# Kernel tuning notes

Hardware: AMD Instinct MI355X
Metric: run time of the kernel (lower is better)

The kernel has to match this reference:

```python
import jax, jax.numpy as jnp
import numpy as np

B, C, H, W = 64, 3, 512, 512
P = 16
D = P * P          # 256 = patch_size**2 (token dim)
GH, GW = H // P, W // P
NP = GH * GW       # 1024 patches
HID = 1024         # FFN hidden
L = 6              # num_layers
NC = 1000          # num_classes
EPS = 1e-5


def setup_inputs() -> dict:
    key = jax.random.key(0)
    ks = jax.random.split(key, 8)
    n = lambda i, shape, scale=0.02: jax.random.normal(ks[i], shape, jnp.float32) * scale
    return dict(
        x=jax.random.normal(ks[0], (B, C, H, W), jnp.float32),
        conv_w=n(1, (D, C, P, P)),
        conv_b=jnp.zeros((D,), jnp.float32),
        pos_emb=n(2, (1, NP + 1, D), 1.0),
        cls_tok=n(3, (1, 1, D), 1.0),
        ln1_s=jnp.ones((L, D), jnp.float32), ln1_b=jnp.zeros((L, D), jnp.float32),
        ln2_s=jnp.ones((L, D), jnp.float32), ln2_b=jnp.zeros((L, D), jnp.float32),
        w1=n(4, (L, D, HID)), b1=jnp.zeros((L, HID), jnp.float32),
        w2=n(5, (L, HID, D)), b2=jnp.zeros((L, D), jnp.float32),
        head_ln_s=jnp.ones((D,), jnp.float32), head_ln_b=jnp.zeros((D,), jnp.float32),
        head_w=n(6, (D, NC)), head_b=jnp.zeros((NC,), jnp.float32),
    )


def _ln(x, s, b):
    m = x.mean(-1, keepdims=True)
    v = ((x - m) ** 2).mean(-1, keepdims=True)
    return (x - m) * jax.lax.rsqrt(v + EPS) * s + b


def reference(x, conv_w, conv_b, pos_emb, cls_tok,
              ln1_s, ln1_b, ln2_s, ln2_b, w1, b1, w2, b2,
              head_ln_s, head_ln_b, head_w, head_b):
    b = x.shape[0]
    # patch-embed conv (kernel==stride) as reshape + einsum
    xr = x.reshape(b, C, GH, P, GW, P)
    tok = jnp.einsum('bchpwq,dcpq->bhwd', xr, conv_w).reshape(b, NP, D) + conv_b
    t = jnp.concatenate([jnp.broadcast_to(cls_tok, (b, 1, D)), tok], axis=1) + pos_emb
    for i in range(L):
        # FNet token mixing: real part of 2D FFT over (tokens, dim)
        h = _ln(t, ln1_s[i], ln1_b[i])
        t = t + jnp.fft.fft2(h, axes=(-2, -1)).real
        # FFN
        h = _ln(t, ln2_s[i], ln2_b[i])
        h = jax.nn.leaky_relu(h @ w1[i] + b1[i], negative_slope=0.01) @ w2[i] + b2[i]
        t = t + h
    pooled = t.mean(axis=1)
    logits = _ln(pooled, head_ln_s, head_ln_b) @ head_w + head_b
    return jax.nn.softmax(logits, axis=-1)
```

## Files before the change

kernel.cpp:

```cpp
#include <hip/hip_runtime.h>
#include <math.h>

#define BATCH 64
#define CIN 3
#define IMH 512
#define IMW 512
#define PSZ 16
#define DIM 256
#define GHN 32
#define GWN 32
#define NTOK 1025
#define HID 1024
#define NLAYER 6
#define NCLS 1000
#define LN_EPS 1e-5f

#define KF 576
#define KR 640
#define MF 144
#define MROWS 65600

typedef __attribute__((ext_vector_type(8))) short short8;
typedef __attribute__((ext_vector_type(4))) float f32x4;

#define MFMA16(acc, a, b) acc = __builtin_amdgcn_mfma_f32_16x16x32_bf16(a, b, acc, 0, 0, 0)

__device__ inline unsigned short rne_bf16(float x) {
    unsigned u = __float_as_uint(x);
    return (unsigned short)((u + 0x7FFF + ((u >> 16) & 1)) >> 16);
}
__device__ inline void split_bf16(float x, unsigned short& hi, unsigned short& lo) {
    unsigned short h = rne_bf16(x);
    hi = h;
    float hf = __uint_as_float((unsigned)h << 16);
    lo = rne_bf16(x - hf);
}
__device__ inline float wave_sum(float v) {
#pragma unroll
    for (int off = 32; off; off >>= 1) v += __shfl_xor(v, off);
    return v;
}
__device__ inline short8 ld8x64(const unsigned short* lds, int row, int q) {
    return *(const short8*)(lds + (row * 8 + (q ^ (row & 7))) * 8);
}
__device__ inline short8 ld8x32(const unsigned short* lds, int row, int q) {
    return *(const short8*)(lds + (row * 4 + (q ^ ((row >> 1) & 3))) * 8);
}
__device__ inline void gl2lds16(const unsigned short* g, unsigned short* l) {
    __builtin_amdgcn_global_load_lds((const __attribute__((address_space(1))) unsigned int*)g,
                                     (__attribute__((address_space(3))) unsigned int*)l, 16, 0, 0);
}
__device__ inline void a_stage128(unsigned short* lds, const unsigned short* g, int lda, int tid, int maxrow) {
    int lane = tid & 63, w = tid >> 6;
#pragma unroll
    for (int s = 0; s < 4; s++) {
        int slot = w * 256 + s * 64;
        int sl = slot + lane;
        int row = sl >> 3, gc = (sl & 7) ^ (row & 7);
        if (row > maxrow) row = maxrow;
        gl2lds16(g + (size_t)row * lda + gc * 8, lds + slot * 8);
    }
}
__device__ inline void a_stage144x32(unsigned short* lds, const unsigned short* g, int lda, int tid) {
    int lane = tid & 63, w = tid >> 6;
#pragma unroll
    for (int s = 0; s < 2; s++) {
        int slot = s * 256 + w * 64;
        int sl = slot + lane;
        int row = sl >> 2, gc = (sl & 3) ^ ((row >> 1) & 3);
        gl2lds16(g + (size_t)row * lda + gc * 8, lds + slot * 8);
    }
    if (w == 0) {
        int slot = 512;
        int sl = slot + lane;
        int row = sl >> 2, gc = (sl & 3) ^ ((row >> 1) & 3);
        gl2lds16(g + (size_t)row * lda + gc * 8, lds + slot * 8);
    }
}

__global__ __launch_bounds__(256) void gen_dft2(unsigned short* C1h, unsigned short* C1l,
                                                unsigned short* S1h, unsigned short* S1l,
                                                unsigned short* C2h, unsigned short* C2l,
                                                unsigned short* S2h, unsigned short* S2l) {
    int idx = blockIdx.x * 256 + threadIdx.x;
    if (idx < KR * KF) {
        int k = idx / KF, n = idx - k * KF;
        float c = 0.f, s = 0.f;
        if (k <= 512 && n <= 512) {
            int r = (k * n) % 1025;
            double ang = 6.283185307179586476925287 * (double)r / 1025.0;
            c = (float)cos(ang); s = (float)sin(ang);
        }
        unsigned short h, l;
        split_bf16(c, h, l); C1h[idx] = h; C1l[idx] = l;
        split_bf16(s, h, l); S1h[idx] = h; S1l[idx] = l;
    }
    if (idx < 256 * 256) {
        int k = idx >> 8, n = idx & 255;
        int r = (k * n) & 255;
        double ang = 6.283185307179586476925287 * (double)r / 256.0;
        float c = (float)cos(ang), s = (float)sin(ang);
        unsigned short h, l;
        split_bf16(c, h, l); C2h[idx] = h; C2l[idx] = l;
        split_bf16(s, h, l); S2h[idx] = h; S2l[idx] = l;
    }
}

__global__ __launch_bounds__(256) void conv_wp(const float* __restrict__ w,
                                               unsigned short* __restrict__ wph, unsigned short* __restrict__ wpl) {
    int idx = blockIdx.x * 256 + threadIdx.x;
    unsigned short h, l;
    split_bf16(w[idx], h, l);
    wph[idx] = h; wpl[idx] = l;
}
__global__ __launch_bounds__(256) void conv_w1t(const float* __restrict__ w1, unsigned short* __restrict__ w1t) {
    int idx = blockIdx.x * 256 + threadIdx.x;
    int l = idx / 262144, rem = idx - l * 262144;
    int n = rem >> 8, k = rem & 255;
    w1t[idx] = rne_bf16(w1[(size_t)l * 262144 + (size_t)k * 1024 + n]);
}
__global__ __launch_bounds__(256) void conv_w2t(const float* __restrict__ w2, unsigned short* __restrict__ w2t) {
    int idx = blockIdx.x * 256 + threadIdx.x;
    int l = idx / 262144, rem = idx - l * 262144;
    int n = rem >> 10, k = rem & 1023;
    w2t[idx] = rne_bf16(w2[(size_t)l * 262144 + (size_t)k * 256 + n]);
}

__global__ __launch_bounds__(256) void cls_init(const float* __restrict__ cls, const float* __restrict__ pos,
                                                float* __restrict__ t) {
    int b = blockIdx.x, tid = threadIdx.x;
    t[(size_t)b * NTOK * DIM + tid] = cls[tid] + pos[tid];
}

__global__ __launch_bounds__(256) void patch_fused(const float* __restrict__ x,
                                                   const unsigned short* __restrict__ wph,
                                                   const unsigned short* __restrict__ wpl,
                                                   const float* __restrict__ cb, const float* __restrict__ pos,
                                                   float* __restrict__ t) {
    __shared__ __align__(16) unsigned short sAh[8192], sAl[8192], sBh[8192], sBl[8192];
    int m0 = blockIdx.x * 128, n0 = blockIdx.y * 128;
    int tid = threadIdx.x, lane = tid & 63, w = tid >> 6;
    int wr = (w >> 1) * 64, wc = (w & 1) * 64;
    f32x4 z = {0.f, 0.f, 0.f, 0.f};
    f32x4 acc[4][4] = {{z, z, z, z}, {z, z, z, z}, {z, z, z, z}, {z, z, z, z}};
    for (int k0 = 0; k0 < 768; k0 += 64) {
#pragma unroll
        for (int s = 0; s < 8; s++) {
            int lin = s * 1024 + tid * 4;
            int row = lin >> 6, kc = lin & 63;
            int m = m0 + row;
            int bb = m >> 10, gh = (m >> 5) & 31, gw = m & 31;
            int k = k0 + kc;
            int c = k >> 8, pp = (k >> 4) & 15, q = k & 15;
            const float* gp = x + (size_t)bb * 786432 + c * 262144 + gh * 8192 + pp * 512 + gw * 16 + q;
            float4 v = *(const float4*)gp;
            ushort4 oh, ol;
            split_bf16(v.x, oh.x, ol.x); split_bf16(v.y, oh.y, ol.y);
            split_bf16(v.z, oh.z, ol.z); split_bf16(v.w, oh.w, ol.w);
            int g = kc >> 3, half = (kc >> 2) & 1;
            int addr = (row * 8 + (g ^ (row & 7))) * 8 + half * 4;
            *(ushort4*)(sAh + addr) = oh;
            *(ushort4*)(sAl + addr) = ol;
        }
        a_stage128(sBh, wph + (size_t)n0 * 768 + k0, 768, tid, 127);
        a_stage128(sBl, wpl + (size_t)n0 * 768 + k0, 768, tid, 127);
        __syncthreads();
#pragma unroll
        for (int kc2 = 0; kc2 < 2; kc2++) {
            int q = (lane >> 4) + kc2 * 4;
            short8 ah[4], al[4], bh8[4], bl8[4];
#pragma unroll
            for (int i = 0; i < 4; i++) {
                ah[i] = ld8x64(sAh, wr + i * 16 + (lane & 15), q);
                al[i] = ld8x64(sAl, wr + i * 16 + (lane & 15), q);
                bh8[i] = ld8x64(sBh, wc + i * 16 + (lane & 15), q);
                bl8[i] = ld8x64(sBl, wc + i * 16 + (lane & 15), q);
            }
#pragma unroll
            for (int i = 0; i < 4; i++)
#pragma unroll
                for (int j = 0; j < 4; j++) {
                    MFMA16(acc[i][j], ah[i], bh8[j]);
                    MFMA16(acc[i][j], ah[i], bl8[j]);
                    MFMA16(acc[i][j], al[i], bh8[j]);
                }
        }
        __syncthreads();
    }
    int q4 = (lane >> 4) * 4;
#pragma unroll
    for (int i = 0; i < 4; i++) {
        int r = m0 + wr + i * 16 + q4;
#pragma unroll
        for (int j = 0; j < 4; j++) {
            int c = n0 + wc + j * 16 + (lane & 15);
#pragma unroll
            for (int g = 0; g < 4; g++) {
                int rr = r + g;
                int bb = rr >> 10, tok = 1 + (rr & 1023);
                t[((size_t)bb * NTOK + tok) * 256 + c] =
                    acc[i][j][g] + cb[c] + pos[(size_t)tok * 256 + c];
            }
        }
    }
}

__global__ __launch_bounds__(256) void ln_stats(const float* __restrict__ t, float2* __restrict__ stats) {
    int wave = threadIdx.x >> 6, lane = threadIdx.x & 63;
    int m = blockIdx.x * 4 + wave;
    const float* row = t + (size_t)m * DIM;
    float4 v = *(const float4*)(row + lane * 4);
    float mean = wave_sum(v.x + v.y + v.z + v.w) * (1.f / 256.f);
    float dx = v.x - mean, dy = v.y - mean, dz = v.z - mean, dw = v.w - mean;
    float sq = wave_sum(dx * dx + dy * dy + dz * dz + dw * dw);
    float rstd = rsqrtf(sq * (1.f / 256.f) + LN_EPS);
    if (lane == 0) stats[m] = make_float2(mean, rstd);
}

__global__ __launch_bounds__(256) void ln2_bf16(const float* __restrict__ t, unsigned short* __restrict__ hh,
                                                const float* __restrict__ s, const float* __restrict__ bb) {
    int wave = threadIdx.x >> 6, lane = threadIdx.x & 63;
    int m = blockIdx.x * 4 + wave;
    const float* row = t + (size_t)m * DIM;
    float4 v = *(const float4*)(row + lane * 4);
    float mean = wave_sum(v.x + v.y + v.z + v.w) * (1.f / 256.f);
    float dx = v.x - mean, dy = v.y - mean, dz = v.z - mean, dw = v.w - mean;
    float sq = wave_sum(dx * dx + dy * dy + dz * dz + dw * dw);
    float rstd = rsqrtf(sq * (1.f / 256.f) + LN_EPS);
    float4 s4 = *(const float4*)(s + lane * 4);
    float4 b4 = *(const float4*)(bb + lane * 4);
    ushort4 o;
    o.x = rne_bf16(dx * rstd * s4.x + b4.x);
    o.y = rne_bf16(dy * rstd * s4.y + b4.y);
    o.z = rne_bf16(dz * rstd * s4.z + b4.z);
    o.w = rne_bf16(dw * rstd * s4.w + b4.w);
    *(ushort4*)(hh + (size_t)m * DIM + lane * 4) = o;
}

__global__ __launch_bounds__(256) void fold_gemm(
    const float* __restrict__ tt, const float2* __restrict__ stats,
    const float* __restrict__ ls, const float* __restrict__ lb,
    const unsigned short* __restrict__ C2h, const unsigned short* __restrict__ C2l,
    const unsigned short* __restrict__ S2h, const unsigned short* __restrict__ S2l,
    unsigned short* __restrict__ Ycth, unsigned short* __restrict__ Yctl,
    unsigned short* __restrict__ Ysth, unsigned short* __restrict__ Ystl) {
    __shared__ __align__(16) unsigned short sAh[4096], sAl[4096], sBh[4608], sBl[4608];
    int m0 = blockIdx.x * 128;
    int zz = blockIdx.y;
    const unsigned short* Bh = zz ? S2h : C2h;
    const unsigned short* Bl = zz ? S2l : C2l;
    unsigned short* Oh = zz ? Ysth : Ycth;
    unsigned short* Ol = zz ? Ystl : Yctl;
    int tid = threadIdx.x, lane = tid & 63, w = tid >> 6;
    int wr = w * 32;
    f32x4 zf = {0.f, 0.f, 0.f, 0.f};
    f32x4 acc[2][9];
#pragma unroll
    for (int i = 0; i < 2; i++)
#pragma unroll
        for (int j = 0; j < 9; j++) acc[i][j] = zf;
    for (int k0 = 0; k0 < 256; k0 += 32) {
#pragma unroll
        for (int s = 0; s < 4; s++) {
            int sl = tid + s * 256;
            int row = sl >> 3, g = sl & 7;
            int r = m0 + row;
            int b = r / KF, np = r - b * KF;
            float4 hv = {0.f, 0.f, 0.f, 0.f};
            if (np <= 512) {
                int d0 = k0 + g * 4;
                float4 s4 = *(const float4*)(ls + d0);
                float4 b4 = *(const float4*)(lb + d0);
                int i1 = b * NTOK + np;
                float2 st1 = stats[i1];
                float4 va = *(const float4*)(tt + (size_t)i1 * 256 + d0);
                float hax = (va.x - st1.x) * st1.y * s4.x + b4.x;
                float hay = (va.y - st1.x) * st1.y * s4.y + b4.y;
                float haz = (va.z - st1.x) * st1.y * s4.z + b4.z;
                float haw = (va.w - st1.x) * st1.y * s4.w + b4.w;
                float hbx = 0.f, hby = 0.f, hbz = 0.f, hbw = 0.f;
                if (np >= 1) {
                    int i2 = b * NTOK + (NTOK - np);
                    float2 st2 = stats[i2];
                    float4 vb = *(const float4*)(tt + (size_t)i2 * 256 + d0);
                    hbx = (vb.x - st2.x) * st2.y * s4.x + b4.x;
                    hby = (vb.y - st2.x) * st2.y * s4.y + b4.y;
                    hbz = (vb.z - st2.x) * st2.y * s4.z + b4.z;
                    hbw = (vb.w - st2.x) * st2.y * s4.w + b4.w;
                }
                if (zz) { hv.x = hax - hbx; hv.y = hay - hby; hv.z = haz - hbz; hv.w = haw - hbw; }
                else    { hv.x = hax + hbx; hv.y = hay + hby; hv.z = haz + hbz; hv.w = haw + hbw; }
            }
            ushort4 oh, ol;
            split_bf16(hv.x, oh.x, ol.x); split_bf16(hv.y, oh.y, ol.y);
            split_bf16(hv.z, oh.z, ol.z); split_bf16(hv.w, oh.w, ol.w);
            int addr = (row * 4 + ((g >> 1) ^ ((row >> 1) & 3))) * 8 + (g & 1) * 4;
            *(ushort4*)(sAh + addr) = oh;
            *(ushort4*)(sAl + addr) = ol;
        }
        a_stage144x32(sBh, Bh + k0, 256, tid);
        a_stage144x32(sBl, Bl + k0, 256, tid);
        __syncthreads();
        int q = lane >> 4;
        short8 ah[2], al[2];
#pragma unroll
        for (int i = 0; i < 2; i++) {
            int r = wr + i * 16 + (lane & 15);
            ah[i] = ld8x32(sAh, r, q); al[i] = ld8x32(sAl, r, q);
        }
#pragma unroll
        for (int j = 0; j < 9; j++) {
            int rb = j * 16 + (lane & 15);
            short8 bh = ld8x32(sBh, rb, q), bl = ld8x32(sBl, rb, q);
#pragma unroll
            for (int i = 0; i < 2; i++) {
                MFMA16(acc[i][j], ah[i], bh);
                MFMA16(acc[i][j], ah[i], bl);
                MFMA16(acc[i][j], al[i], bh);
            }
        }
        __syncthreads();
    }
    int q4 = (lane >> 4) * 4;
#pragma unroll
    for (int i = 0; i < 2; i++) {
        int r = m0 + wr + i * 16 + q4;
        int bidx = r / KF, kp = r - bidx * KF;
#pragma unroll
        for (int j = 0; j < 9; j++) {
            int c = j * 16 + (lane & 15);
            ushort4 oh, ol;
            split_bf16(acc[i][j][0], oh.x, ol.x);
            split_bf16(acc[i][j][1], oh.y, ol.y);
            split_bf16(acc[i][j][2], oh.z, ol.z);
            split_bf16(acc[i][j][3], oh.w, ol.w);
            size_t off = ((size_t)bidx * MF + c) * KF + kp;
            *(ushort4*)(Oh + off) = oh;
            *(ushort4*)(Ol + off) = ol;
        }
    }
}

__global__ __launch_bounds__(512, 6) void fft_big_dual(
    const unsigned short* __restrict__ C1h, const unsigned short* __restrict__ C1l,
    const unsigned short* __restrict__ S1h, const unsigned short* __restrict__ S1l,
    const unsigned short* __restrict__ Ych, const unsigned short* __restrict__ Ycl,
    const unsigned short* __restrict__ Ysh, const unsigned short* __restrict__ Ysl,
    float* __restrict__ t) {
    __shared__ __align__(16) unsigned short sC1h[4096], sC1l[4096], sS1h[4096], sS1l[4096];
    __shared__ __align__(16) unsigned short sYch[2048], sYcl[2048], sYsh[2048], sYsl[2048];
    int k0m = blockIdx.x * 128, n0 = blockIdx.y * 64;
    int tid = threadIdx.x, lane = tid & 63, w = tid >> 6;
    int wr = (w >> 1) * 32, wc = (w & 1) * 32;
    f32x4 z = {0.f, 0.f, 0.f, 0.f};
    f32x4 U[2][2], V[2][2];
#pragma unroll
    for (int i = 0; i < 2; i++)
#pragma unroll
        for (int j = 0; j < 2; j++) { U[i][j] = z; V[i][j] = z; }
    for (int kk0 = 0; kk0 < KF; kk0 += 32) {
        {
            int row = tid >> 2, gc = (tid & 3) ^ ((row >> 1) & 3);
            size_t ga = (size_t)k0m * KF + kk0 + (size_t)row * KF + gc * 8;
            unsigned short* lbase0 = sC1h + (size_t)(w * 64) * 8;
            unsigned short* lbase1 = sC1l + (size_t)(w * 64) * 8;
            unsigned short* lbase2 = sS1h + (size_t)(w * 64) * 8;
            unsigned short* lbase3 = sS1l + (size_t)(w * 64) * 8;
            gl2lds16(C1h + ga, lbase0);
            gl2lds16(C1l + ga, lbase1);
            gl2lds16(S1h + ga, lbase2);
            gl2lds16(S1l + ga, lbase3);
        }
        {
            int m = w >> 1, p = w & 1;
            const unsigned short* yg;
            unsigned short* yl;
            if (m == 0)      { yg = Ych; yl = sYch; }
            else if (m == 1) { yg = Ycl; yl = sYcl; }
            else if (m == 2) { yg = Ysh; yl = sYsh; }
            else             { yg = Ysl; yl = sYsl; }
            size_t gb = (size_t)n0 * KF + kk0;
#pragma unroll
            for (int s = 0; s < 2; s++) {
                int slot = p * 128 + s * 64;
                int sl = slot + lane;
                int row = sl >> 2, gc = (sl & 3) ^ ((row >> 1) & 3);
                gl2lds16(yg + gb + (size_t)row * KF + gc * 8, yl + slot * 8);
            }
        }
        __syncthreads();
        int q = lane >> 4;
        short8 bch[2], bcl[2], bsh[2], bsl[2];
#pragma unroll
        for (int j = 0; j < 2; j++) {
            int r2 = wc + j * 16 + (lane & 15);
            bch[j] = ld8x32(sYch, r2, q); bcl[j] = ld8x32(sYcl, r2, q);
            bsh[j] = ld8x32(sYsh, r2, q); bsl[j] = ld8x32(sYsl, r2, q);
        }
#pragma unroll
        for (int i = 0; i < 2; i++) {
            int r1 = wr + i * 16 + (lane & 15);
            short8 ach = ld8x32(sC1h, r1, q), acl = ld8x32(sC1l, r1, q);
            short8 ash = ld8x32(sS1h, r1, q), asl = ld8x32(sS1l, r1, q);
#pragma unroll
            for (int j = 0; j < 2; j++) {
                MFMA16(U[i][j], ach, bch[j]);
                MFMA16(U[i][j], ach, bcl[j]);
                MFMA16(U[i][j], acl, bch[j]);
                MFMA16(V[i][j], ash, bsh[j]);
                MFMA16(V[i][j], ash, bsl[j]);
                MFMA16(V[i][j], asl, bsh[j]);
            }
        }
        __syncthreads();
    }
    int q4 = (lane >> 4) * 4;
#pragma unroll
    for (int j = 0; j < 2; j++) {
        int rcol = n0 + wc + j * 16 + (lane & 15);
        int b = rcol / MF, mm = rcol - b * MF;
        float* tb = t + (size_t)b * NTOK * DIM;
        if (mm > 128) continue;
#pragma unroll
        for (int i = 0; i < 2; i++) {
            int kk = k0m + wr + i * 16 + q4;
#pragma unroll
            for (int g = 0; g < 4; g++) {
                int k = kk + g;
                if (k > 512) continue;
                float u = U[i][j][g], v = V[i][j][g];
                tb[(size_t)k * 256 + mm] += u - v;
                if (mm >= 1 && mm <= 127) tb[(size_t)k * 256 + 256 - mm] += u + v;
                if (k >= 1) {
                    tb[(size_t)(NTOK - k) * 256 + mm] += u + v;
                    if (mm >= 1 && mm <= 127) tb[(size_t)(NTOK - k) * 256 + 256 - mm] += u - v;
                }
            }
        }
    }
}

__global__ __launch_bounds__(256) void gemm_ffn1(
    const unsigned short* __restrict__ A, const unsigned short* __restrict__ Bt,
    const float* __restrict__ b1, unsigned short* __restrict__ Hid) {
    __shared__ __align__(16) unsigned short sA[8192], sB[8192];
    int m0 = blockIdx.x * 128, n0 = blockIdx.y * 128;
    int tid = threadIdx.x, lane = tid & 63, w = tid >> 6;
    int wr = (w >> 1) * 64, wc = (w & 1) * 64;
    int maxrow = MROWS - 1 - m0; if (maxrow > 127) maxrow = 127;
    f32x4 z = {0.f, 0.f, 0.f, 0.f};
    f32x4 acc[4][4] = {{z, z, z, z}, {z, z, z, z}, {z, z, z, z}, {z, z, z, z}};
    for (int k0 = 0; k0 < 256; k0 += 64) {
        a_stage128(sA, A + (size_t)m0 * 256 + k0, 256, tid, maxrow);
        a_stage128(sB, Bt + (size_t)n0 * 256 + k0, 256, tid, 127);
        __syncthreads();
#pragma unroll
        for (int kc = 0; kc < 2; kc++) {
            int q = (lane >> 4) + kc * 4;
            short8 a8[4], b8[4];
#pragma unroll
            for (int i = 0; i < 4; i++) {
                a8[i] = ld8x64(sA, wr + i * 16 + (lane & 15), q);
                b8[i] = ld8x64(sB, wc + i * 16 + (lane & 15), q);
            }
#pragma unroll
            for (int i = 0; i < 4; i++)
#pragma unroll
                for (int j = 0; j < 4; j++) MFMA16(acc[i][j], a8[i], b8[j]);
        }
        __syncthreads();
    }
    int q4 = (lane >> 4) * 4;
#pragma unroll
    for (int i = 0; i < 4; i++) {
        int r = m0 + wr + i * 16 + q4;
#pragma unroll
        for (int j = 0; j < 4; j++) {
            int c = n0 + wc + j * 16 + (lane & 15);
            float bv = b1[c];
#pragma unroll
            for (int g = 0; g < 4; g++) {
                int rr = r + g;
                if (rr < MROWS) {
                    float val = acc[i][j][g] + bv;
                    val = val > 0.f ? val : 0.01f * val;
                    Hid[(size_t)rr * 1024 + c] = rne_bf16(val);
                }
            }
        }
    }
}

__global__ __launch_bounds__(256) void gemm_ffn2(
    const unsigned short* __restrict__ A, const unsigned short* __restrict__ Bt,
    const float* __restrict__ b2, float* __restrict__ t) {
    __shared__ __align__(16) unsigned short sA[8192], sB[8192];
    int m0 = blockIdx.x * 128, n0 = blockIdx.y * 128;
    int tid = threadIdx.x, lane = tid & 63, w = tid >> 6;
    int wr = (w >> 1) * 64, wc = (w & 1) * 64;
    int maxrow = MROWS - 1 - m0; if (maxrow > 127) maxrow = 127;
    f32x4 z = {0.f, 0.f, 0.f, 0.f};
    f32x4 acc[4][4] = {{z, z, z, z}, {z, z, z, z}, {z, z, z, z}, {z, z, z, z}};
    for (int k0 = 0; k0 < 1024; k0 += 64) {
        a_stage128(sA, A + (size_t)m0 * 1024 + k0, 1024, tid, maxrow);
        a_stage128(sB, Bt + (size_t)n0 * 1024 + k0, 1024, tid, 127);
        __syncthreads();
#pragma unroll
        for (int kc = 0; kc < 2; kc++) {
            int q = (lane >> 4) + kc * 4;
            short8 a8[4], b8[4];
#pragma unroll
            for (int i = 0; i < 4; i++) {
                a8[i] = ld8x64(sA, wr + i * 16 + (lane & 15), q);
                b8[i] = ld8x64(sB, wc + i * 16 + (lane & 15), q);
            }
#pragma unroll
            for (int i = 0; i < 4; i++)
#pragma unroll
                for (int j = 0; j < 4; j++) MFMA16(acc[i][j], a8[i], b8[j]);
        }
        __syncthreads();
    }
    int q4 = (lane >> 4) * 4;
#pragma unroll
    for (int i = 0; i < 4; i++) {
        int r = m0 + wr + i * 16 + q4;
#pragma unroll
        for (int j = 0; j < 4; j++) {
            int c = n0 + wc + j * 16 + (lane & 15);
            float bv = b2[c];
#pragma unroll
            for (int g = 0; g < 4; g++) {
                int rr = r + g;
                if (rr < MROWS) t[(size_t)rr * 256 + c] += acc[i][j][g] + bv;
            }
        }
    }
}

__global__ __launch_bounds__(256) void head_kernel(const float* __restrict__ t,
                                                   const float* __restrict__ hs, const float* __restrict__ hb,
                                                   const float* __restrict__ hw, const float* __restrict__ hbias,
                                                   float* __restrict__ out) {
    __shared__ float red[256];
    __shared__ float lnv[256];
    int b = blockIdx.x, tid = threadIdx.x;
    const float* tb = t + (size_t)b * NTOK * DIM;
    float s = 0.f;
    for (int m = 0; m < NTOK; m++) s += tb[m * DIM + tid];
    s *= (1.f / 1025.f);
    red[tid] = s;
    __syncthreads();
    for (int off = 128; off; off >>= 1) {
        if (tid < off) red[tid] += red[tid + off];
        __syncthreads();
    }
    float mean = red[0] * (1.f / 256.f);
    __syncthreads();
    float d = s - mean;
    red[tid] = d * d;
    __syncthreads();
    for (int off = 128; off; off >>= 1) {
        if (tid < off) red[tid] += red[tid + off];
        __syncthreads();
    }
    float rstd = rsqrtf(red[0] * (1.f / 256.f) + LN_EPS);
    __syncthreads();
    lnv[tid] = d * rstd * hs[tid] + hb[tid];
    __syncthreads();
    float lo[4];
#pragma unroll
    for (int jj = 0; jj < 4; jj++) {
        int n = tid + jj * 256;
        float a = -1e30f;
        if (n < NCLS) {
            a = hbias[n];
            for (int dd = 0; dd < DIM; dd++) a += lnv[dd] * hw[dd * NCLS + n];
        }
        lo[jj] = a;
    }
    float mx = fmaxf(fmaxf(lo[0], lo[1]), fmaxf(lo[2], lo[3]));
    red[tid] = mx;
    __syncthreads();
    for (int off = 128; off; off >>= 1) {
        if (tid < off) red[tid] = fmaxf(red[tid], red[tid + off]);
        __syncthreads();
    }
    float gmax = red[0];
    __syncthreads();
    float ev[4];
    float es = 0.f;
#pragma unroll
    for (int jj = 0; jj < 4; jj++) {
        int n = tid + jj * 256;
        ev[jj] = 0.f;
        if (n < NCLS) {
            ev[jj] = expf(lo[jj] - gmax);
            es += ev[jj];
        }
    }
    red[tid] = es;
    __syncthreads();
    for (int off = 128; off; off >>= 1) {
        if (tid < off) red[tid] += red[tid + off];
        __syncthreads();
    }
    float inv = 1.f / red[0];
#pragma unroll
    for (int jj = 0; jj < 4; jj++) {
        int n = tid + jj * 256;
        if (n < NCLS) out[(size_t)b * NCLS + n] = ev[jj] * inv;
    }
}

extern "C" void kernel_launch(void* const* d_in, const int* in_sizes, int n_in,
                              void* d_out, int out_size, void* d_ws, size_t ws_size,
                              hipStream_t stream) {
    const float* x      = (const float*)d_in[0];
    const float* conv_w = (const float*)d_in[1];
    const float* conv_b = (const float*)d_in[2];
    const float* pos    = (const float*)d_in[3];
    const float* cls    = (const float*)d_in[4];
    const float* ln1_s  = (const float*)d_in[5];
    const float* ln1_b  = (const float*)d_in[6];
    const float* ln2_s  = (const float*)d_in[7];
    const float* ln2_b  = (const float*)d_in[8];
    const float* w1     = (const float*)d_in[9];
    const float* b1     = (const float*)d_in[10];
    const float* w2     = (const float*)d_in[11];
    const float* b2     = (const float*)d_in[12];
    const float* hls    = (const float*)d_in[13];
    const float* hlb    = (const float*)d_in[14];
    const float* hw     = (const float*)d_in[15];
    const float* hbias  = (const float*)d_in[16];
    float* out = (float*)d_out;
    char* W = (char*)d_ws;

    float*          t    = (float*)(W + 0ULL);
    char*           pool = W + 67174400ULL;
    unsigned short* Ycth = (unsigned short*)(pool + 75497472ULL);
    unsigned short* Yctl = (unsigned short*)(pool + 75497472ULL + 10616832ULL);
    unsigned short* Ysth = (unsigned short*)(pool + 75497472ULL + 2 * 10616832ULL);
    unsigned short* Ystl = (unsigned short*)(pool + 75497472ULL + 3 * 10616832ULL);
    unsigned short* Hid  = (unsigned short*)(pool);
    unsigned short* hh   = (unsigned short*)(pool + 134348800ULL);
    unsigned short* C1h  = (unsigned short*)(W + 235110400ULL);
    unsigned short* C1l  = (unsigned short*)(W + 235110400ULL + 737280ULL);
    unsigned short* S1h  = (unsigned short*)(W + 235110400ULL + 2 * 737280ULL);
    unsigned short* S1l  = (unsigned short*)(W + 235110400ULL + 3 * 737280ULL);
    unsigned short* C2h  = (unsigned short*)(W + 238059520ULL);
    unsigned short* C2l  = (unsigned short*)(W + 238059520ULL + 131072ULL);
    unsigned short* S2h  = (unsigned short*)(W + 238059520ULL + 2 * 131072ULL);
    unsigned short* S2l  = (unsigned short*)(W + 238059520ULL + 3 * 131072ULL);
    unsigned short* w1t  = (unsigned short*)(W + 238583808ULL);
    unsigned short* w2t  = (unsigned short*)(W + 241729536ULL);
    unsigned short* wph  = (unsigned short*)(W + 244875264ULL);
    unsigned short* wpl  = (unsigned short*)(W + 245268480ULL);
    float2*         stats = (float2*)(W + 245661696ULL);

    gen_dft2<<<dim3(1440), dim3(256), 0, stream>>>(C1h, C1l, S1h, S1l, C2h, C2l, S2h, S2l);
    conv_wp<<<dim3(768), dim3(256), 0, stream>>>(conv_w, wph, wpl);
    conv_w1t<<<dim3(6144), dim3(256), 0, stream>>>(w1, w1t);
    conv_w2t<<<dim3(6144), dim3(256), 0, stream>>>(w2, w2t);
    cls_init<<<dim3(BATCH), dim3(256), 0, stream>>>(cls, pos, t);
    patch_fused<<<dim3(512, 2), dim3(256), 0, stream>>>(x, wph, wpl, conv_b, pos, t);

    for (int l = 0; l < NLAYER; l++) {
        ln_stats<<<dim3(16400), dim3(256), 0, stream>>>(t, stats);
        fold_gemm<<<dim3(288, 2), dim3(256), 0, stream>>>(
            t, stats, ln1_s + l * DIM, ln1_b + l * DIM,
            C2h, C2l, S2h, S2l, Ycth, Yctl, Ysth, Ystl);
        fft_big_dual<<<dim3(5, 144), dim3(512), 0, stream>>>(
            C1h, C1l, S1h, S1l, Ycth, Yctl, Ysth, Ystl, t);
        ln2_bf16<<<dim3(16400), dim3(256), 0, stream>>>(t, hh, ln2_s + l * DIM, ln2_b + l * DIM);
        gemm_ffn1<<<dim3(513, 8), dim3(256), 0, stream>>>(
            hh, w1t + (size_t)l * 262144, b1 + (size_t)l * HID, Hid);
        gemm_ffn2<<<dim3(513, 2), dim3(256), 0, stream>>>(
            Hid, w2t + (size_t)l * 262144, b2 + (size_t)l * DIM, t);
    }
    head_kernel<<<dim3(BATCH), dim3(256), 0, stream>>>(t, hls, hlb, hw, hbias, out);
}
```

Baseline: 2.969 ms.

## Fuse FFN GEMMs into one kernel keeping hidden activations in LDS; shrink patch K-tile

Replaces the two FFN GEMM kernels with one 512-thread kernel per 128-row tile. It computes each 128-wide hidden chunk, applies bias and leaky ReLU, stores it as bf16 in LDS, and immediately accumulates the second GEMM, so the 65600x1024 hidden tensor never goes to global memory. The patch-embed GEMM also moves to a 32-wide K step with half-size LDS buffers, likely to free shared memory and raise occupancy. The trade-off is only 513 blocks with heavy LDS use (~96KB) and more syncs per block, which may lower occupancy and overlap.

```diff
diff --git a/kernel.cpp b/kernel.cpp
--- a/kernel.cpp
+++ b/kernel.cpp
@@ -61,6 +61,27 @@
         gl2lds16(g + (size_t)row * lda + gc * 8, lds + slot * 8);
     }
 }
+__device__ inline void a_stage128_512(unsigned short* lds, const unsigned short* g, int lda, int tid, int maxrow) {
+    int lane = tid & 63, w = tid >> 6;
+#pragma unroll
+    for (int s = 0; s < 2; s++) {
+        int slot = w * 128 + s * 64;
+        int sl = slot + lane;
+        int row = sl >> 3, gc = (sl & 7) ^ (row & 7);
+        if (row > maxrow) row = maxrow;
+        gl2lds16(g + (size_t)row * lda + gc * 8, lds + slot * 8);
+    }
+}
+__device__ inline void b_stage128x32(unsigned short* lds, const unsigned short* g, int lda, int tid) {
+    int lane = tid & 63;
+#pragma unroll
+    for (int s = 0; s < 2; s++) {
+        int slot = s * 256 + (tid >> 6) * 64;
+        int sl = slot + lane;
+        int row = sl >> 2, gc = (sl & 3) ^ ((row >> 1) & 3);
+        gl2lds16(g + (size_t)row * lda + gc * 8, lds + slot * 8);
+    }
+}
 __device__ inline void a_stage144x32(unsigned short* lds, const unsigned short* g, int lda, int tid) {
     int lane = tid & 63, w = tid >> 6;
 #pragma unroll
@@ -137,17 +158,17 @@
                                                    const unsigned short* __restrict__ wpl,
                                                    const float* __restrict__ cb, const float* __restrict__ pos,
                                                    float* __restrict__ t) {
-    __shared__ __align__(16) unsigned short sAh[8192], sAl[8192], sBh[8192], sBl[8192];
+    __shared__ __align__(16) unsigned short sAh[4096], sAl[4096], sBh[4096], sBl[4096];
     int m0 = blockIdx.x * 128, n0 = blockIdx.y * 128;
     int tid = threadIdx.x, lane = tid & 63, w = tid >> 6;
     int wr = (w >> 1) * 64, wc = (w & 1) * 64;
     f32x4 z = {0.f, 0.f, 0.f, 0.f};
     f32x4 acc[4][4] = {{z, z, z, z}, {z, z, z, z}, {z, z, z, z}, {z, z, z, z}};
-    for (int k0 = 0; k0 < 768; k0 += 64) {
-#pragma unroll
-        for (int s = 0; s < 8; s++) {
+    for (int k0 = 0; k0 < 768; k0 += 32) {
+#pragma unroll
+        for (int s = 0; s < 4; s++) {
             int lin = s * 1024 + tid * 4;
-            int row = lin >> 6, kc = lin & 63;
+            int row = lin >> 5, kc = lin & 31;
             int m = m0 + row;
             int bb = m >> 10, gh = (m >> 5) & 31, gw = m & 31;
             int k = k0 + kc;
@@ -158,33 +179,30 @@
             split_bf16(v.x, oh.x, ol.x); split_bf16(v.y, oh.y, ol.y);
             split_bf16(v.z, oh.z, ol.z); split_bf16(v.w, oh.w, ol.w);
             int g = kc >> 3, half = (kc >> 2) & 1;
-            int addr = (row * 8 + (g ^ (row & 7))) * 8 + half * 4;
+            int addr = (row * 4 + (g ^ ((row >> 1) & 3))) * 8 + half * 4;
             *(ushort4*)(sAh + addr) = oh;
             *(ushort4*)(sAl + addr) = ol;
         }
-        a_stage128(sBh, wph + (size_t)n0 * 768 + k0, 768, tid, 127);
-        a_stage128(sBl, wpl + (size_t)n0 * 768 + k0, 768, tid, 127);
-        __syncthreads();
-#pragma unroll
-        for (int kc2 = 0; kc2 < 2; kc2++) {
-            int q = (lane >> 4) + kc2 * 4;
-            short8 ah[4], al[4], bh8[4], bl8[4];
-#pragma unroll
-            for (int i = 0; i < 4; i++) {
-                ah[i] = ld8x64(sAh, wr + i * 16 + (lane & 15), q);
-                al[i] = ld8x64(sAl, wr + i * 16 + (lane & 15), q);
-                bh8[i] = ld8x64(sBh, wc + i * 16 + (lane & 15), q);
-                bl8[i] = ld8x64(sBl, wc + i * 16 + (lane & 15), q);
-            }
-#pragma unroll
-            for (int i = 0; i < 4; i++)
-#pragma unroll
-                for (int j = 0; j < 4; j++) {
-                    MFMA16(acc[i][j], ah[i], bh8[j]);
-                    MFMA16(acc[i][j], ah[i], bl8[j]);
-                    MFMA16(acc[i][j], al[i], bh8[j]);
-                }
-        }
+        b_stage128x32(sBh, wph + (size_t)n0 * 768 + k0, 768, tid);
+        b_stage128x32(sBl, wpl + (size_t)n0 * 768 + k0, 768, tid);
+        __syncthreads();
+        int q = lane >> 4;
+        short8 ah[4], al[4], bh8[4], bl8[4];
+#pragma unroll
+        for (int i = 0; i < 4; i++) {
+            ah[i] = ld8x32(sAh, wr + i * 16 + (lane & 15), q);
+            al[i] = ld8x32(sAl, wr + i * 16 + (lane & 15), q);
+            bh8[i] = ld8x32(sBh, wc + i * 16 + (lane & 15), q);
+            bl8[i] = ld8x32(sBl, wc + i * 16 + (lane & 15), q);
+        }
+#pragma unroll
+        for (int i = 0; i < 4; i++)
+#pragma unroll
+            for (int j = 0; j < 4; j++) {
+                MFMA16(acc[i][j], ah[i], bh8[j]);
+                MFMA16(acc[i][j], ah[i], bl8[j]);
+                MFMA16(acc[i][j], al[i], bh8[j]);
+            }
         __syncthreads();
     }
     int q4 = (lane >> 4) * 4;
@@ -440,99 +458,105 @@
     }
 }
 
-__global__ __launch_bounds__(256) void gemm_ffn1(
-    const unsigned short* __restrict__ A, const unsigned short* __restrict__ Bt,
-    const float* __restrict__ b1, unsigned short* __restrict__ Hid) {
-    __shared__ __align__(16) unsigned short sA[8192], sB[8192];
-    int m0 = blockIdx.x * 128, n0 = blockIdx.y * 128;
+__global__ __launch_bounds__(512) void gemm_ffn_fused(
+    const unsigned short* __restrict__ A, const unsigned short* __restrict__ W1t,
+    const float* __restrict__ b1, const unsigned short* __restrict__ W2t,
+    const float* __restrict__ b2, float* __restrict__ t) {
+    __shared__ __align__(16) unsigned short sB[32768];
+    __shared__ __align__(16) unsigned short sH[16384];
+    int m0 = blockIdx.x * 128;
     int tid = threadIdx.x, lane = tid & 63, w = tid >> 6;
-    int wr = (w >> 1) * 64, wc = (w & 1) * 64;
-    int maxrow = MROWS - 1 - m0; if (maxrow > 127) maxrow = 127;
+    int wr1 = (w >> 1) * 32, wc1 = (w & 1) * 64;
+    int wr2 = (w >> 2) * 64, wc2 = (w & 3) * 64;
+    short8 areg[2][8];
+#pragma unroll
+    for (int i = 0; i < 2; i++) {
+        int rr = m0 + wr1 + i * 16 + (lane & 15);
+        if (rr > MROWS - 1) rr = MROWS - 1;
+        const unsigned short* ap = A + (size_t)rr * 256 + (lane >> 4) * 8;
+#pragma unroll
+        for (int p = 0; p < 4; p++)
+#pragma unroll
+            for (int kc = 0; kc < 2; kc++)
+                areg[i][p * 2 + kc] = *(const short8*)(ap + p * 64 + kc * 32);
+    }
     f32x4 z = {0.f, 0.f, 0.f, 0.f};
-    f32x4 acc[4][4] = {{z, z, z, z}, {z, z, z, z}, {z, z, z, z}, {z, z, z, z}};
-    for (int k0 = 0; k0 < 256; k0 += 64) {
-        a_stage128(sA, A + (size_t)m0 * 256 + k0, 256, tid, maxrow);
-        a_stage128(sB, Bt + (size_t)n0 * 256 + k0, 256, tid, 127);
-        __syncthreads();
-#pragma unroll
-        for (int kc = 0; kc < 2; kc++) {
-            int q = (lane >> 4) + kc * 4;
-            short8 a8[4], b8[4];
-#pragma unroll
-            for (int i = 0; i < 4; i++) {
-                a8[i] = ld8x64(sA, wr + i * 16 + (lane & 15), q);
-                b8[i] = ld8x64(sB, wc + i * 16 + (lane & 15), q);
-            }
-#pragma unroll
-            for (int i = 0; i < 4; i++)
-#pragma unroll
-                for (int j = 0; j < 4; j++) MFMA16(acc[i][j], a8[i], b8[j]);
-        }
-        __syncthreads();
-    }
+    f32x4 acc2[4][4] = {{z, z, z, z}, {z, z, z, z}, {z, z, z, z}, {z, z, z, z}};
     int q4 = (lane >> 4) * 4;
+    for (int hc = 0; hc < 8; hc++) {
+        int h0 = hc * 128;
+        __syncthreads();
+#pragma unroll
+        for (int p = 0; p < 4; p++)
+            a_stage128_512(sB + p * 8192, W1t + (size_t)h0 * 256 + p * 64, 256, tid, 127);
+        __syncthreads();
+        f32x4 acc1[2][4] = {{z, z, z, z}, {z, z, z, z}};
+#pragma unroll
+        for (int p = 0; p < 4; p++)
+#pragma unroll
+            for (int kc = 0; kc < 2; kc++) {
+                int q = (lane >> 4) + kc * 4;
+                short8 bh[4];
+#pragma unroll
+                for (int j = 0; j < 4; j++)
+                    bh[j] = ld8x64(sB + p * 8192, wc1 + j * 16 + (lane & 15), q);
+#pragma unroll
+                for (int i = 0; i < 2; i++)
+#pragma unroll
+                    for (int j = 0; j < 4; j++) MFMA16(acc1[i][j], areg[i][p * 2 + kc], bh[j]);
+            }
+#pragma unroll
+        for (int j = 0; j < 4; j++) {
+            int col = wc1 + j * 16 + (lane & 15);
+            float bv = b1[h0 + col];
+            int panel = col >> 6, c64 = col & 63;
+#pragma unroll
+            for (int i = 0; i < 2; i++)
+#pragma unroll
+                for (int g = 0; g < 4; g++) {
+                    int row = wr1 + i * 16 + q4 + g;
+                    float val = acc1[i][j][g] + bv;
+                    val = val > 0.f ? val : 0.01f * val;
+                    sH[panel * 8192 + (row * 8 + ((c64 >> 3) ^ (row & 7))) * 8 + (c64 & 7)] = rne_bf16(val);
+                }
+        }
+        __syncthreads();
+#pragma unroll
+        for (int hp = 0; hp < 2; hp++)
+#pragma unroll
+            for (int rb = 0; rb < 2; rb++)
+                a_stage128_512(sB + hp * 16384 + rb * 8192,
+                               W2t + (size_t)(rb * 128) * 1024 + h0 + hp * 64, 1024, tid, 127);
+        __syncthreads();
+#pragma unroll
+        for (int hp = 0; hp < 2; hp++)
+#pragma unroll
+            for (int kc = 0; kc < 2; kc++) {
+                int q = (lane >> 4) + kc * 4;
+                short8 ah[4], bh[4];
+#pragma unroll
+                for (int i = 0; i < 4; i++)
+                    ah[i] = ld8x64(sH + hp * 8192, wr2 + i * 16 + (lane & 15), q);
+#pragma unroll
+                for (int j = 0; j < 4; j++)
+                    bh[j] = ld8x64(sB + hp * 16384, wc2 + j * 16 + (lane & 15), q);
+#pragma unroll
+                for (int i = 0; i < 4; i++)
+#pragma unroll
+                    for (int j = 0; j < 4; j++) MFMA16(acc2[i][j], ah[i], bh[j]);
+            }
+    }
 #pragma unroll
     for (int i = 0; i < 4; i++) {
-        int r = m0 + wr + i * 16 + q4;
+        int r = m0 + wr2 + i * 16 + q4;
 #pragma unroll
         for (int j = 0; j < 4; j++) {
-            int c = n0 + wc + j * 16 + (lane & 15);
-            float bv = b1[c];
+            int c = wc2 + j * 16 + (lane & 15);
+            float bv = b2[c];
 #pragma unroll
             for (int g = 0; g < 4; g++) {
                 int rr = r + g;
-                if (rr < MROWS) {
-                    float val = acc[i][j][g] + bv;
-                    val = val > 0.f ? val : 0.01f * val;
-                    Hid[(size_t)rr * 1024 + c] = rne_bf16(val);
-                }
-            }
-        }
-    }
-}
-
-__global__ __launch_bounds__(256) void gemm_ffn2(
-    const unsigned short* __restrict__ A, const unsigned short* __restrict__ Bt,
-    const float* __restrict__ b2, float* __restrict__ t) {
-    __shared__ __align__(16) unsigned short sA[8192], sB[8192];
-    int m0 = blockIdx.x * 128, n0 = blockIdx.y * 128;
-    int tid = threadIdx.x, lane = tid & 63, w = tid >> 6;
-    int wr = (w >> 1) * 64, wc = (w & 1) * 64;
-    int maxrow = MROWS - 1 - m0; if (maxrow > 127) maxrow = 127;
-    f32x4 z = {0.f, 0.f, 0.f, 0.f};
-    f32x4 acc[4][4] = {{z, z, z, z}, {z, z, z, z}, {z, z, z, z}, {z, z, z, z}};
-    for (int k0 = 0; k0 < 1024; k0 += 64) {
-        a_stage128(sA, A + (size_t)m0 * 1024 + k0, 1024, tid, maxrow);
-        a_stage128(sB, Bt + (size_t)n0 * 1024 + k0, 1024, tid, 127);
-        __syncthreads();
-#pragma unroll
-        for (int kc = 0; kc < 2; kc++) {
-            int q = (lane >> 4) + kc * 4;
-            short8 a8[4], b8[4];
-#pragma unroll
-            for (int i = 0; i < 4; i++) {
-                a8[i] = ld8x64(sA, wr + i * 16 + (lane & 15), q);
-                b8[i] = ld8x64(sB, wc + i * 16 + (lane & 15), q);
-            }
-#pragma unroll
-            for (int i = 0; i < 4; i++)
-#pragma unroll
-                for (int j = 0; j < 4; j++) MFMA16(acc[i][j], a8[i], b8[j]);
-        }
-        __syncthreads();
-    }
-    int q4 = (lane >> 4) * 4;
-#pragma unroll
-    for (int i = 0; i < 4; i++) {
-        int r = m0 + wr + i * 16 + q4;
-#pragma unroll
-        for (int j = 0; j < 4; j++) {
-            int c = n0 + wc + j * 16 + (lane & 15);
-            float bv = b2[c];
-#pragma unroll
-            for (int g = 0; g < 4; g++) {
-                int rr = r + g;
-                if (rr < MROWS) t[(size_t)rr * 256 + c] += acc[i][j][g] + bv;
+                if (rr < MROWS) t[(size_t)rr * 256 + c] += acc2[i][j][g] + bv;
             }
         }
     }
@@ -642,7 +666,6 @@
     unsigned short* Yctl = (unsigned short*)(pool + 75497472ULL + 10616832ULL);
     unsigned short* Ysth = (unsigned short*)(pool + 75497472ULL + 2 * 10616832ULL);
     unsigned short* Ystl = (unsigned short*)(pool + 75497472ULL + 3 * 10616832ULL);
-    unsigned short* Hid  = (unsigned short*)(pool);
     unsigned short* hh   = (unsigned short*)(pool + 134348800ULL);
     unsigned short* C1h  = (unsigned short*)(W + 235110400ULL);
     unsigned short* C1l  = (unsigned short*)(W + 235110400ULL + 737280ULL);
@@ -673,10 +696,9 @@
         fft_big_dual<<<dim3(5, 144), dim3(512), 0, stream>>>(
             C1h, C1l, S1h, S1l, Ycth, Yctl, Ysth, Ystl, t);
         ln2_bf16<<<dim3(16400), dim3(256), 0, stream>>>(t, hh, ln2_s + l * DIM, ln2_b + l * DIM);
-        gemm_ffn1<<<dim3(513, 8), dim3(256), 0, stream>>>(
-            hh, w1t + (size_t)l * 262144, b1 + (size_t)l * HID, Hid);
-        gemm_ffn2<<<dim3(513, 2), dim3(256), 0, stream>>>(
-            Hid, w2t + (size_t)l * 262144, b2 + (size_t)l * DIM, t);
+        gemm_ffn_fused<<<dim3(513), dim3(512), 0, stream>>>(
+            hh, w1t + (size_t)l * 262144, b1 + (size_t)l * HID,
+            w2t + (size_t)l * 262144, b2 + (size_t)l * DIM, t);
     }
     head_kernel<<<dim3(BATCH), dim3(256), 0, stream>>>(t, hls, hlb, hw, hbias, out);
 }
```

Result: faster. 2.735 ms (-7.9%).
